# Kernel tuning notes

Hardware: AMD Instinct MI355X
Metric: run time of the kernel (lower is better)

Reference implementation:

```python
import jax, jax.numpy as jnp
import numpy as np

B, S, D = 4, 2048, 1024
H = 16
HD = D // H  # 64

def setup_inputs() -> dict:
    key = jax.random.key(0)
    k1, k2, k3 = jax.random.split(key, 3)
    x = jax.random.normal(k1, (B, S, D), dtype=jnp.float32)
    w_qkv = jax.random.normal(k2, (D, 3 * D), dtype=jnp.float32) * 0.02
    w_proj = jax.random.normal(k3, (D, D), dtype=jnp.float32) * 0.02
    return {"x": x, "w_qkv": w_qkv, "w_proj": w_proj}

def reference(x, w_qkv, w_proj):
    b, s, d = x.shape
    qkv = x @ w_qkv                                  # [b,s,3d]
    q, k, v = jnp.split(qkv, 3, axis=2)
    # [b,s,d] -> [b,h,s,hd]
    q = q.reshape(b, s, H, HD).transpose(0, 2, 1, 3)
    k = k.reshape(b, s, H, HD).transpose(0, 2, 1, 3)
    v = v.reshape(b, s, H, HD).transpose(0, 2, 1, 3)
    att = jnp.einsum('bhqd,bhkd->bhqk', q, k) / jnp.sqrt(jnp.float32(HD))
    causal = jnp.tril(jnp.ones((s, s), dtype=bool))
    att = jnp.where(causal[None, None], att, jnp.float32(-jnp.inf))
    att = jax.nn.softmax(att, axis=-1)
    y = jnp.einsum('bhqk,bhkd->bhqd', att, v)        # [b,h,s,hd]
    y = y.transpose(0, 2, 1, 3).reshape(b, s, d)
    return y @ w_proj
```

## Files before the change

kernel.cpp:

```cpp
#include <hip/hip_runtime.h>
#include <stdint.h>

typedef unsigned short u16;
typedef __attribute__((ext_vector_type(8))) short bf16x8;
typedef __attribute__((ext_vector_type(4))) float f32x4;

__device__ __forceinline__ u16 f2bf(float f) {
  union { float f; unsigned u; } v; v.f = f;
  unsigned r = v.u + 0x7fffu + ((v.u >> 16) & 1u);
  return (u16)(r >> 16);
}

__device__ __forceinline__ void async_copy16(u16* lds_dst, const u16* g_src) {
  __builtin_amdgcn_global_load_lds(
      (const __attribute__((address_space(1))) unsigned*)(g_src),
      (__attribute__((address_space(3))) unsigned*)(lds_dst),
      16, 0, 0);
}

__global__ void cvt_bf16_kernel(const float* __restrict__ in, u16* __restrict__ out, int n4) {
  int i = blockIdx.x * blockDim.x + threadIdx.x;
  int stride = gridDim.x * blockDim.x;
  for (; i < n4; i += stride) {
    float4 v = ((const float4*)in)[i];
    ushort4 o;
    o.x = f2bf(v.x); o.y = f2bf(v.y); o.z = f2bf(v.z); o.w = f2bf(v.w);
    ((ushort4*)out)[i] = o;
  }
}

__global__ void transpose_cvt_kernel(const float* __restrict__ in, u16* __restrict__ out,
                                     int R, int C) {
  __shared__ float tile[32][33];
  int bx = blockIdx.x * 32;
  int by = blockIdx.y * 32;
  int tx = threadIdx.x & 31, ty = threadIdx.x >> 5;
#pragma unroll
  for (int j = 0; j < 32; j += 8)
    tile[ty + j][tx] = in[(size_t)(by + ty + j) * C + bx + tx];
  __syncthreads();
#pragma unroll
  for (int j = 0; j < 32; j += 8)
    out[(size_t)(bx + ty + j) * R + by + tx] = f2bf(tile[tx][ty + j]);
}

template<int MODE>
__global__ __launch_bounds__(256, 2)
void gemm_bt(const u16* __restrict__ A, const u16* __restrict__ BT,
             int K, int N,
             u16* __restrict__ q_o, u16* __restrict__ k_o, u16* __restrict__ vt_o,
             float* __restrict__ f_o) {
  __shared__ u16 As[128 * 32];
  __shared__ u16 Bs[128 * 32];
  const int t = threadIdx.x;
  const int w = t >> 6, l = t & 63;
  const int lr = l & 15, lk = (l >> 4) * 8;
  const int m0 = blockIdx.x * 128, n0 = blockIdx.y * 128;
  const int wr = (w >> 1) * 64, wc = (w & 1) * 64;
  f32x4 acc[4][4] = {};
  const int row_s = t >> 2, seg_s = (t & 3) * 8;

  for (int kk = 0; kk < K; kk += 32) {
    async_copy16(&As[t * 8],         &A[(size_t)(m0 + row_s) * K + kk + seg_s]);
    async_copy16(&As[(t + 256) * 8], &A[(size_t)(m0 + row_s + 64) * K + kk + seg_s]);
    async_copy16(&Bs[t * 8],         &BT[(size_t)(n0 + row_s) * K + kk + seg_s]);
    async_copy16(&Bs[(t + 256) * 8], &BT[(size_t)(n0 + row_s + 64) * K + kk + seg_s]);
    __syncthreads();
    bf16x8 af[4], bfr[4];
#pragma unroll
    for (int mf = 0; mf < 4; ++mf)
      af[mf] = *(const bf16x8*)&As[(wr + mf * 16 + lr) * 32 + lk];
#pragma unroll
    for (int nf = 0; nf < 4; ++nf)
      bfr[nf] = *(const bf16x8*)&Bs[(wc + nf * 16 + lr) * 32 + lk];
#pragma unroll
    for (int mf = 0; mf < 4; ++mf)
#pragma unroll
      for (int nf = 0; nf < 4; ++nf)
        acc[mf][nf] = __builtin_amdgcn_mfma_f32_16x16x32_bf16(af[mf], bfr[nf], acc[mf][nf], 0, 0, 0);
    __syncthreads();
  }

#pragma unroll
  for (int mf = 0; mf < 4; ++mf) {
#pragma unroll
    for (int nf = 0; nf < 4; ++nf) {
      const int col = n0 + wc + nf * 16 + lr;
#pragma unroll
      for (int j = 0; j < 4; ++j) {
        const int row = m0 + wr + mf * 16 + ((l >> 4) << 2) + j;
        const float v = acc[mf][nf][j];
        if (MODE == 0) {
          const int which = col >> 10, r = col & 1023;
          const int h = r >> 6, hd = r & 63;
          const int b = row >> 11, s = row & 2047;
          const size_t bh = (size_t)b * 16 + h;
          if (which == 0)      q_o[(bh * 2048 + s) * 64 + hd] = f2bf(v * 0.125f);
          else if (which == 1) k_o[(bh * 2048 + s) * 64 + hd] = f2bf(v);
          else                 vt_o[(bh * 64 + hd) * 2048 + s] = f2bf(v);
        } else {
          f_o[(size_t)row * N + col] = v;
        }
      }
    }
  }
}

__global__ __launch_bounds__(256, 2)
void attn_kernel(const u16* __restrict__ qws, const u16* __restrict__ kws,
                 const u16* __restrict__ vtws, u16* __restrict__ ybf) {
  __shared__ u16 Ksh[2][64 * 64];
  __shared__ u16 VTsh[2][64 * 64];
  __shared__ u16 Psh[4][32 * 64];

  const int bh = blockIdx.x & 63;
  const int qtile = 15 - (blockIdx.x >> 6);
  const int t = threadIdx.x;
  const int w = t >> 6, l = t & 63;
  const int lr = l & 15, g = l >> 4;
  const int q0 = qtile * 128 + w * 32;

  bf16x8 qf[2][2];
#pragma unroll
  for (int mf = 0; mf < 2; ++mf) {
    const u16* qb = qws + ((size_t)bh * 2048 + q0 + mf * 16 + lr) * 64 + g * 8;
#pragma unroll
    for (int ks = 0; ks < 2; ++ks) qf[mf][ks] = *(const bf16x8*)(qb + ks * 32);
  }

  f32x4 oacc[2][4] = {};
  float lrun[2][4] = {};

  const int srow = t >> 3;
  const int ssw = ((t & 7) * 16) ^ ((srow & 7) << 4);
  const u16* kb0 = kws + ((size_t)bh * 2048 + srow) * 64 + (ssw >> 1);
  const u16* vb0 = vtws + ((size_t)bh * 64 + srow) * 2048 + (ssw >> 1);

#define STAGE(kv0, buf)                                                \
  do {                                                                 \
    async_copy16(&Ksh[buf][t * 8],          kb0 + (size_t)(kv0)*64);   \
    async_copy16(&Ksh[buf][(t + 256) * 8],  kb0 + (size_t)((kv0)+32)*64); \
    async_copy16(&VTsh[buf][t * 8],         vb0 + (kv0));              \
    async_copy16(&VTsh[buf][(t + 256) * 8], vb0 + (size_t)32*2048 + (kv0)); \
  } while (0)

  const int nt = (qtile + 1) * 2;
  STAGE(0, 0);
  __syncthreads();

  for (int ti = 0; ti < nt; ++ti) {
    const int kv0 = ti * 64;
    const int cur = ti & 1;
    if (ti + 1 < nt) STAGE((ti + 1) * 64, cur ^ 1);

    if (kv0 <= q0 + 31) {
      const u16* Kc = Ksh[cur];
      const u16* Vc = VTsh[cur];

      f32x4 s[2][4] = {};
      __builtin_amdgcn_s_setprio(1);
#pragma unroll
      for (int f = 0; f < 4; ++f) {
        const int krow = f * 16 + lr;
        const int kswz = (krow & 7) << 4;
#pragma unroll
        for (int ks = 0; ks < 2; ++ks) {
          bf16x8 kb = *(const bf16x8*)&Kc[krow * 64 + (((ks * 64 + g * 16) ^ kswz) >> 1)];
          s[0][f] = __builtin_amdgcn_mfma_f32_16x16x32_bf16(qf[0][ks], kb, s[0][f], 0, 0, 0);
          s[1][f] = __builtin_amdgcn_mfma_f32_16x16x32_bf16(qf[1][ks], kb, s[1][f], 0, 0, 0);
        }
      }
      __builtin_amdgcn_s_setprio(0);

      const bool diag = (kv0 + 63 > q0);
#pragma unroll
      for (int mf = 0; mf < 2; ++mf)
#pragma unroll
        for (int f = 0; f < 4; ++f)
#pragma unroll
          for (int j = 0; j < 4; ++j) {
            float p = __expf(s[mf][f][j]);
            if (diag) {
              const int key = kv0 + f * 16 + lr;
              const int qrow = q0 + mf * 16 + g * 4 + j;
              p = (key <= qrow) ? p : 0.f;
            }
            s[mf][f][j] = p;
            lrun[mf][j] += p;
          }

#pragma unroll
      for (int mf = 0; mf < 2; ++mf)
#pragma unroll
        for (int f = 0; f < 4; ++f)
#pragma unroll
          for (int j = 0; j < 4; ++j) {
            const int prow = mf * 16 + g * 4 + j;
            Psh[w][prow * 64 + (((f * 32 + lr * 2) ^ ((prow & 7) << 4)) >> 1)] =
                f2bf(s[mf][f][j]);
          }

#pragma unroll
      for (int ks = 0; ks < 2; ++ks) {
        bf16x8 pa[2];
#pragma unroll
        for (int mf = 0; mf < 2; ++mf) {
          const int prow = mf * 16 + lr;
          pa[mf] = *(const bf16x8*)&Psh[w][prow * 64 + (((ks * 64 + g * 16) ^ ((prow & 7) << 4)) >> 1)];
        }
        __builtin_amdgcn_s_setprio(1);
#pragma unroll
        for (int nf = 0; nf < 4; ++nf) {
          const int vrow = nf * 16 + lr;
          bf16x8 vb = *(const bf16x8*)&Vc[vrow * 64 + (((ks * 64 + g * 16) ^ ((vrow & 7) << 4)) >> 1)];
          oacc[0][nf] = __builtin_amdgcn_mfma_f32_16x16x32_bf16(pa[0], vb, oacc[0][nf], 0, 0, 0);
          oacc[1][nf] = __builtin_amdgcn_mfma_f32_16x16x32_bf16(pa[1], vb, oacc[1][nf], 0, 0, 0);
        }
        __builtin_amdgcn_s_setprio(0);
      }
    }
    __syncthreads();
  }
#undef STAGE

  float linv[2][4];
#pragma unroll
  for (int mf = 0; mf < 2; ++mf)
#pragma unroll
    for (int j = 0; j < 4; ++j) {
      float s = lrun[mf][j];
#pragma unroll
      for (int d = 1; d < 16; d <<= 1) s += __shfl_xor(s, d, 64);
      linv[mf][j] = 1.f / s;
    }

  const int b = bh >> 4, h = bh & 15;
#pragma unroll
  for (int mf = 0; mf < 2; ++mf)
#pragma unroll
    for (int nf = 0; nf < 4; ++nf) {
      const int col = nf * 16 + lr;
#pragma unroll
      for (int j = 0; j < 4; ++j) {
        const int row = q0 + mf * 16 + g * 4 + j;
        const float o = oacc[mf][nf][j] * linv[mf][j];
        ybf[((size_t)b * 2048 + row) * 1024 + h * 64 + col] = f2bf(o);
      }
    }
}

extern "C" void kernel_launch(void* const* d_in, const int* in_sizes, int n_in,
                              void* d_out, int out_size, void* d_ws, size_t ws_size,
                              hipStream_t stream) {
  const float* x     = (const float*)d_in[0];
  const float* wqkv  = (const float*)d_in[1];
  const float* wproj = (const float*)d_in[2];
  float* out = (float*)d_out;

  char* ws = (char*)d_ws;
  u16* xbf    = (u16*)ws;
  u16* ybf    = xbf;
  u16* wqkvT  = (u16*)(ws + 16777216);
  u16* wprojT = (u16*)(ws + 16777216 + 6291456);
  u16* qws    = (u16*)(ws + 25165824);
  u16* kws    = (u16*)(ws + 41943040);
  u16* vtws   = (u16*)(ws + 58720256);

  cvt_bf16_kernel<<<2048, 256, 0, stream>>>(x, xbf, (8192 * 1024) / 4);
  transpose_cvt_kernel<<<dim3(3072 / 32, 1024 / 32), 256, 0, stream>>>(wqkv, wqkvT, 1024, 3072);
  transpose_cvt_kernel<<<dim3(1024 / 32, 1024 / 32), 256, 0, stream>>>(wproj, wprojT, 1024, 1024);
  gemm_bt<0><<<dim3(64, 24), 256, 0, stream>>>(xbf, wqkvT, 1024, 3072, qws, kws, vtws, nullptr);
  attn_kernel<<<16 * 64, 256, 0, stream>>>(qws, kws, vtws, ybf);
  gemm_bt<1><<<dim3(64, 8), 256, 0, stream>>>(ybf, wprojT, 1024, 1024, nullptr, nullptr, nullptr, out);
}
```

Measured before the change: 188.5 us.

## Add 256x256-tile 8-wave pipelined GEMM for the QKV projection

Replaces the 128x128 single-stage QKV GEMM with a 512-thread kernel that computes 256x256 tiles. It uses a 64-wide K step, double-buffered swizzled LDS, and async global-to-LDS prefetch interleaved with MFMA phases under explicit barriers and waitcnts. The aim is higher data reuse per LDS load and overlap of memory traffic with matrix math. In exchange it needs 128KB of LDS per block, so occupancy drops to one block per CU. The 384-block grid also leaves a partial second wave. The output projection keeps the old kernel, which is simplified to its float-output path.

```diff
diff --git a/kernel.cpp b/kernel.cpp
--- a/kernel.cpp
+++ b/kernel.cpp
@@ -17,6 +17,8 @@
       (__attribute__((address_space(3))) unsigned*)(lds_dst),
       16, 0, 0);
 }
+
+#define MFMA16(a, b, c) __builtin_amdgcn_mfma_f32_16x16x32_bf16((a), (b), (c), 0, 0, 0)
 
 __global__ void cvt_bf16_kernel(const float* __restrict__ in, u16* __restrict__ out, int n4) {
   int i = blockIdx.x * blockDim.x + threadIdx.x;
@@ -45,11 +47,168 @@
 }
 
 template<int MODE>
+__global__ __launch_bounds__(512, 2)
+void gemm256(const u16* __restrict__ A, const u16* __restrict__ BT,
+             int N,
+             u16* __restrict__ q_o, u16* __restrict__ k_o, u16* __restrict__ vt_o,
+             float* __restrict__ f_o) {
+  constexpr int K = 1024;
+  constexpr int NT = K / 64;
+  __shared__ u16 AsF[2 * 2 * 8192];
+  __shared__ u16 BsF[2 * 2 * 8192];
+
+  const int t = threadIdx.x;
+  const int w = t >> 6, l = t & 63;
+  const int lr = l & 15, g = l >> 4;
+  const int wm = w >> 2, wn = w & 3;
+  const int m0 = blockIdx.x * 256, n0 = blockIdx.y * 256;
+
+  const int r = t >> 3;
+  const int sw = ((t & 7) * 16) ^ ((r & 7) << 4);
+  const u16* pA0 = A + (size_t)(m0 + r) * K + (sw >> 1);
+  const u16* pA1 = pA0 + (size_t)128 * K;
+  const u16* pB0 = BT + (size_t)(n0 + r) * K + (sw >> 1);
+  const u16* pB1 = pB0 + (size_t)128 * K;
+
+#define STG(ptr, dstbase)                                            \
+  do {                                                               \
+    async_copy16((dstbase) + t * 8, (ptr));                          \
+    async_copy16((dstbase) + 4096 + t * 8, (ptr) + (size_t)64 * K);  \
+  } while (0)
+
+  f32x4 acc[8][4] = {};
+
+  STG(pA0, AsF);
+  STG(pA1, AsF + 8192);
+  STG(pB0, BsF);
+  STG(pB1, BsF + 8192);
+  STG(pA0 + 64, AsF + 2 * 8192);
+  STG(pA1 + 64, AsF + 3 * 8192);
+  asm volatile("s_waitcnt vmcnt(4)" ::: "memory");
+  asm volatile("s_barrier" ::: "memory");
+
+  const int brow0 = (wn & 1) * 64;
+  for (int T = 0; T < NT; ++T) {
+    const int b = T & 1;
+    const u16* Ab = AsF + (b * 2 + wm) * 8192;
+    const u16* Bb = BsF + (b * 2 + (wn >> 1)) * 8192;
+    bf16x8 a03[4][2], a47[4][2], bb[4][2];
+
+#pragma unroll
+    for (int mf = 0; mf < 4; ++mf)
+#pragma unroll
+      for (int ks = 0; ks < 2; ++ks) {
+        const int row = mf * 16 + lr;
+        a03[mf][ks] = *(const bf16x8*)&Ab[row * 64 + (((ks * 64 + g * 16) ^ ((row & 7) << 4)) >> 1)];
+      }
+#pragma unroll
+    for (int nf = 0; nf < 2; ++nf)
+#pragma unroll
+      for (int ks = 0; ks < 2; ++ks) {
+        const int row = brow0 + nf * 16 + lr;
+        bb[nf][ks] = *(const bf16x8*)&Bb[row * 64 + (((ks * 64 + g * 16) ^ ((row & 7) << 4)) >> 1)];
+      }
+    if (T < NT - 1) STG(pB0 + (T + 1) * 64, BsF + ((T + 1) & 1) * 2 * 8192);
+    asm volatile("s_barrier" ::: "memory");
+    __builtin_amdgcn_s_setprio(1);
+#pragma unroll
+    for (int mf = 0; mf < 4; ++mf)
+#pragma unroll
+      for (int nf = 0; nf < 2; ++nf) {
+        acc[mf][nf] = MFMA16(a03[mf][0], bb[nf][0], acc[mf][nf]);
+        acc[mf][nf] = MFMA16(a03[mf][1], bb[nf][1], acc[mf][nf]);
+      }
+    __builtin_amdgcn_s_setprio(0);
+    asm volatile("s_barrier" ::: "memory");
+
+#pragma unroll
+    for (int mf = 0; mf < 4; ++mf)
+#pragma unroll
+      for (int ks = 0; ks < 2; ++ks) {
+        const int row = 64 + mf * 16 + lr;
+        a47[mf][ks] = *(const bf16x8*)&Ab[row * 64 + (((ks * 64 + g * 16) ^ ((row & 7) << 4)) >> 1)];
+      }
+#pragma unroll
+    for (int nf = 2; nf < 4; ++nf)
+#pragma unroll
+      for (int ks = 0; ks < 2; ++ks) {
+        const int row = brow0 + nf * 16 + lr;
+        bb[nf][ks] = *(const bf16x8*)&Bb[row * 64 + (((ks * 64 + g * 16) ^ ((row & 7) << 4)) >> 1)];
+      }
+    if (T < NT - 1) STG(pB1 + (T + 1) * 64, BsF + (((T + 1) & 1) * 2 + 1) * 8192);
+    asm volatile("s_barrier" ::: "memory");
+    __builtin_amdgcn_s_setprio(1);
+#pragma unroll
+    for (int mf = 0; mf < 4; ++mf)
+#pragma unroll
+      for (int nf = 2; nf < 4; ++nf) {
+        acc[mf][nf] = MFMA16(a03[mf][0], bb[nf][0], acc[mf][nf]);
+        acc[mf][nf] = MFMA16(a03[mf][1], bb[nf][1], acc[mf][nf]);
+      }
+    __builtin_amdgcn_s_setprio(0);
+    asm volatile("s_waitcnt lgkmcnt(0)" ::: "memory");
+    asm volatile("s_barrier" ::: "memory");
+
+    if (T < NT - 2) STG(pA0 + (T + 2) * 64, AsF + b * 2 * 8192);
+    asm volatile("s_barrier" ::: "memory");
+    __builtin_amdgcn_s_setprio(1);
+#pragma unroll
+    for (int mf = 0; mf < 4; ++mf)
+#pragma unroll
+      for (int nf = 0; nf < 2; ++nf) {
+        acc[4 + mf][nf] = MFMA16(a47[mf][0], bb[nf][0], acc[4 + mf][nf]);
+        acc[4 + mf][nf] = MFMA16(a47[mf][1], bb[nf][1], acc[4 + mf][nf]);
+      }
+    __builtin_amdgcn_s_setprio(0);
+    asm volatile("s_barrier" ::: "memory");
+
+    if (T < NT - 2) STG(pA1 + (T + 2) * 64, AsF + (b * 2 + 1) * 8192);
+    asm volatile("s_barrier" ::: "memory");
+    __builtin_amdgcn_s_setprio(1);
+#pragma unroll
+    for (int mf = 0; mf < 4; ++mf)
+#pragma unroll
+      for (int nf = 2; nf < 4; ++nf) {
+        acc[4 + mf][nf] = MFMA16(a47[mf][0], bb[nf][0], acc[4 + mf][nf]);
+        acc[4 + mf][nf] = MFMA16(a47[mf][1], bb[nf][1], acc[4 + mf][nf]);
+      }
+    __builtin_amdgcn_s_setprio(0);
+    if (T < NT - 2)
+      asm volatile("s_waitcnt vmcnt(4)" ::: "memory");
+    else if (T == NT - 2)
+      asm volatile("s_waitcnt vmcnt(0)" ::: "memory");
+    asm volatile("s_barrier" ::: "memory");
+  }
+#undef STG
+
+#pragma unroll
+  for (int mf = 0; mf < 8; ++mf) {
+#pragma unroll
+    for (int nf = 0; nf < 4; ++nf) {
+      const int col = n0 + wn * 64 + nf * 16 + lr;
+#pragma unroll
+      for (int j = 0; j < 4; ++j) {
+        const int row = m0 + wm * 128 + mf * 16 + g * 4 + j;
+        const float v = acc[mf][nf][j];
+        if (MODE == 0) {
+          const int which = col >> 10, rr = col & 1023;
+          const int h = rr >> 6, hd = rr & 63;
+          const int bb_ = row >> 11, s = row & 2047;
+          const size_t bh = (size_t)bb_ * 16 + h;
+          if (which == 0)      q_o[(bh * 2048 + s) * 64 + hd] = f2bf(v * 0.125f);
+          else if (which == 1) k_o[(bh * 2048 + s) * 64 + hd] = f2bf(v);
+          else                 vt_o[(bh * 64 + hd) * 2048 + s] = f2bf(v);
+        } else {
+          f_o[(size_t)row * N + col] = v;
+        }
+      }
+    }
+  }
+}
+
 __global__ __launch_bounds__(256, 2)
 void gemm_bt(const u16* __restrict__ A, const u16* __restrict__ BT,
-             int K, int N,
-             u16* __restrict__ q_o, u16* __restrict__ k_o, u16* __restrict__ vt_o,
-             float* __restrict__ f_o) {
+             int K, int N, float* __restrict__ f_o) {
   __shared__ u16 As[128 * 32];
   __shared__ u16 Bs[128 * 32];
   const int t = threadIdx.x;
@@ -77,33 +236,21 @@
     for (int mf = 0; mf < 4; ++mf)
 #pragma unroll
       for (int nf = 0; nf < 4; ++nf)
-        acc[mf][nf] = __builtin_amdgcn_mfma_f32_16x16x32_bf16(af[mf], bfr[nf], acc[mf][nf], 0, 0, 0);
+        acc[mf][nf] = MFMA16(af[mf], bfr[nf], acc[mf][nf]);
     __syncthreads();
   }
 
 #pragma unroll
-  for (int mf = 0; mf < 4; ++mf) {
+  for (int mf = 0; mf < 4; ++mf)
 #pragma unroll
     for (int nf = 0; nf < 4; ++nf) {
       const int col = n0 + wc + nf * 16 + lr;
 #pragma unroll
       for (int j = 0; j < 4; ++j) {
         const int row = m0 + wr + mf * 16 + ((l >> 4) << 2) + j;
-        const float v = acc[mf][nf][j];
-        if (MODE == 0) {
-          const int which = col >> 10, r = col & 1023;
-          const int h = r >> 6, hd = r & 63;
-          const int b = row >> 11, s = row & 2047;
-          const size_t bh = (size_t)b * 16 + h;
-          if (which == 0)      q_o[(bh * 2048 + s) * 64 + hd] = f2bf(v * 0.125f);
-          else if (which == 1) k_o[(bh * 2048 + s) * 64 + hd] = f2bf(v);
-          else                 vt_o[(bh * 64 + hd) * 2048 + s] = f2bf(v);
-        } else {
-          f_o[(size_t)row * N + col] = v;
-        }
+        f_o[(size_t)row * N + col] = acc[mf][nf][j];
       }
     }
-  }
 }
 
 __global__ __launch_bounds__(256, 2)
@@ -166,8 +313,8 @@
 #pragma unroll
         for (int ks = 0; ks < 2; ++ks) {
           bf16x8 kb = *(const bf16x8*)&Kc[krow * 64 + (((ks * 64 + g * 16) ^ kswz) >> 1)];
-          s[0][f] = __builtin_amdgcn_mfma_f32_16x16x32_bf16(qf[0][ks], kb, s[0][f], 0, 0, 0);
-          s[1][f] = __builtin_amdgcn_mfma_f32_16x16x32_bf16(qf[1][ks], kb, s[1][f], 0, 0, 0);
+          s[0][f] = MFMA16(qf[0][ks], kb, s[0][f]);
+          s[1][f] = MFMA16(qf[1][ks], kb, s[1][f]);
         }
       }
       __builtin_amdgcn_s_setprio(0);
@@ -213,8 +360,8 @@
         for (int nf = 0; nf < 4; ++nf) {
           const int vrow = nf * 16 + lr;
           bf16x8 vb = *(const bf16x8*)&Vc[vrow * 64 + (((ks * 64 + g * 16) ^ ((vrow & 7) << 4)) >> 1)];
-          oacc[0][nf] = __builtin_amdgcn_mfma_f32_16x16x32_bf16(pa[0], vb, oacc[0][nf], 0, 0, 0);
-          oacc[1][nf] = __builtin_amdgcn_mfma_f32_16x16x32_bf16(pa[1], vb, oacc[1][nf], 0, 0, 0);
+          oacc[0][nf] = MFMA16(pa[0], vb, oacc[0][nf]);
+          oacc[1][nf] = MFMA16(pa[1], vb, oacc[1][nf]);
         }
         __builtin_amdgcn_s_setprio(0);
       }
@@ -269,7 +416,7 @@
   cvt_bf16_kernel<<<2048, 256, 0, stream>>>(x, xbf, (8192 * 1024) / 4);
   transpose_cvt_kernel<<<dim3(3072 / 32, 1024 / 32), 256, 0, stream>>>(wqkv, wqkvT, 1024, 3072);
   transpose_cvt_kernel<<<dim3(1024 / 32, 1024 / 32), 256, 0, stream>>>(wproj, wprojT, 1024, 1024);
-  gemm_bt<0><<<dim3(64, 24), 256, 0, stream>>>(xbf, wqkvT, 1024, 3072, qws, kws, vtws, nullptr);
+  gemm256<0><<<dim3(32, 12), 512, 0, stream>>>(xbf, wqkvT, 3072, qws, kws, vtws, nullptr);
   attn_kernel<<<16 * 64, 256, 0, stream>>>(qws, kws, vtws, ybf);
-  gemm_bt<1><<<dim3(64, 8), 256, 0, stream>>>(ybf, wprojT, 1024, 1024, nullptr, nullptr, nullptr, out);
-}
+  gemm_bt<<<dim3(64, 8), 256, 0, stream>>>(ybf, wprojT, 1024, 1024, out);
+}
```

New measurement: 196.9 us. 4.5% more time.

## Double-buffer GEMM LDS tiles with K=64 stages and XOR-swizzled layout

Applied to the files above, without the earlier changes.

Rewrites the projection GEMM main loop to use two LDS buffers holding 64-wide K tiles, issuing the async global-to-LDS copy for the next tile while MFMAs run on the current one. This cuts the loop to one barrier per iteration instead of two and halves the iteration count. The shared tile is XOR-swizzled per row to avoid LDS bank conflicts on fragment reads. LDS use grows to 64KB per block, which may limit occupancy to the two blocks requested by the launch bounds.

```diff
diff --git a/kernel.cpp b/kernel.cpp
--- a/kernel.cpp
+++ b/kernel.cpp
@@ -17,6 +17,8 @@
       (__attribute__((address_space(3))) unsigned*)(lds_dst),
       16, 0, 0);
 }
+
+#define MFMA16(a, b, c) __builtin_amdgcn_mfma_f32_16x16x32_bf16((a), (b), (c), 0, 0, 0)
 
 __global__ void cvt_bf16_kernel(const float* __restrict__ in, u16* __restrict__ out, int n4) {
   int i = blockIdx.x * blockDim.x + threadIdx.x;
@@ -46,53 +48,84 @@
 
 template<int MODE>
 __global__ __launch_bounds__(256, 2)
-void gemm_bt(const u16* __restrict__ A, const u16* __restrict__ BT,
+void gemm2ph(const u16* __restrict__ A, const u16* __restrict__ BT,
              int K, int N,
              u16* __restrict__ q_o, u16* __restrict__ k_o, u16* __restrict__ vt_o,
              float* __restrict__ f_o) {
-  __shared__ u16 As[128 * 32];
-  __shared__ u16 Bs[128 * 32];
+  __shared__ u16 As[2][128 * 64];
+  __shared__ u16 Bs[2][128 * 64];
+
   const int t = threadIdx.x;
   const int w = t >> 6, l = t & 63;
-  const int lr = l & 15, lk = (l >> 4) * 8;
+  const int lr = l & 15, g = l >> 4;
+  const int wm = (w >> 1) * 64, wn = (w & 1) * 64;
   const int m0 = blockIdx.x * 128, n0 = blockIdx.y * 128;
-  const int wr = (w >> 1) * 64, wc = (w & 1) * 64;
+
+  const int r = t >> 3;
+  const int sw = ((t & 7) * 16) ^ ((r & 7) << 4);
+  const u16* pA = A + (size_t)(m0 + r) * K + (sw >> 1);
+  const u16* pB = BT + (size_t)(n0 + r) * K + (sw >> 1);
+
+#define STG(buf, kk)                                                    \
+  do {                                                                  \
+    async_copy16(&As[buf][t * 8],        pA + (kk));                    \
+    async_copy16(&As[buf][2048 + t * 8], pA + (size_t)32 * K + (kk));   \
+    async_copy16(&As[buf][4096 + t * 8], pA + (size_t)64 * K + (kk));   \
+    async_copy16(&As[buf][6144 + t * 8], pA + (size_t)96 * K + (kk));   \
+    async_copy16(&Bs[buf][t * 8],        pB + (kk));                    \
+    async_copy16(&Bs[buf][2048 + t * 8], pB + (size_t)32 * K + (kk));   \
+    async_copy16(&Bs[buf][4096 + t * 8], pB + (size_t)64 * K + (kk));   \
+    async_copy16(&Bs[buf][6144 + t * 8], pB + (size_t)96 * K + (kk));   \
+  } while (0)
+
   f32x4 acc[4][4] = {};
-  const int row_s = t >> 2, seg_s = (t & 3) * 8;
-
-  for (int kk = 0; kk < K; kk += 32) {
-    async_copy16(&As[t * 8],         &A[(size_t)(m0 + row_s) * K + kk + seg_s]);
-    async_copy16(&As[(t + 256) * 8], &A[(size_t)(m0 + row_s + 64) * K + kk + seg_s]);
-    async_copy16(&Bs[t * 8],         &BT[(size_t)(n0 + row_s) * K + kk + seg_s]);
-    async_copy16(&Bs[(t + 256) * 8], &BT[(size_t)(n0 + row_s + 64) * K + kk + seg_s]);
+
+  STG(0, 0);
+  __syncthreads();
+
+  const int NTt = K / 64;
+  for (int T = 0; T < NTt; ++T) {
+    const int cur = T & 1;
+    if (T + 1 < NTt) STG(cur ^ 1, (T + 1) * 64);
+
+    bf16x8 af[4][2], bfr[4][2];
+#pragma unroll
+    for (int mf = 0; mf < 4; ++mf)
+#pragma unroll
+      for (int ks = 0; ks < 2; ++ks) {
+        const int row = wm + mf * 16 + lr;
+        af[mf][ks] = *(const bf16x8*)&As[cur][row * 64 + (((ks * 64 + g * 16) ^ ((row & 7) << 4)) >> 1)];
+      }
+#pragma unroll
+    for (int nf = 0; nf < 4; ++nf)
+#pragma unroll
+      for (int ks = 0; ks < 2; ++ks) {
+        const int row = wn + nf * 16 + lr;
+        bfr[nf][ks] = *(const bf16x8*)&Bs[cur][row * 64 + (((ks * 64 + g * 16) ^ ((row & 7) << 4)) >> 1)];
+      }
+#pragma unroll
+    for (int mf = 0; mf < 4; ++mf)
+#pragma unroll
+      for (int nf = 0; nf < 4; ++nf) {
+        acc[mf][nf] = MFMA16(af[mf][0], bfr[nf][0], acc[mf][nf]);
+        acc[mf][nf] = MFMA16(af[mf][1], bfr[nf][1], acc[mf][nf]);
+      }
     __syncthreads();
-    bf16x8 af[4], bfr[4];
-#pragma unroll
-    for (int mf = 0; mf < 4; ++mf)
-      af[mf] = *(const bf16x8*)&As[(wr + mf * 16 + lr) * 32 + lk];
-#pragma unroll
-    for (int nf = 0; nf < 4; ++nf)
-      bfr[nf] = *(const bf16x8*)&Bs[(wc + nf * 16 + lr) * 32 + lk];
-#pragma unroll
-    for (int mf = 0; mf < 4; ++mf)
-#pragma unroll
-      for (int nf = 0; nf < 4; ++nf)
-        acc[mf][nf] = __builtin_amdgcn_mfma_f32_16x16x32_bf16(af[mf], bfr[nf], acc[mf][nf], 0, 0, 0);
-    __syncthreads();
-  }
+  }
+#undef STG
 
 #pragma unroll
   for (int mf = 0; mf < 4; ++mf) {
 #pragma unroll
     for (int nf = 0; nf < 4; ++nf) {
-      const int col = n0 + wc + nf * 16 + lr;
+      const int col = n0 + wn + nf * 16 + lr;
 #pragma unroll
       for (int j = 0; j < 4; ++j) {
-        const int row = m0 + wr + mf * 16 + ((l >> 4) << 2) + j;
+        const int row = m0 + wm + mf * 16 + g * 4 + j;
         const float v = acc[mf][nf][j];
         if (MODE == 0) {
-          const int which = col >> 10, r = col & 1023;
-          const int h = r >> 6, hd = r & 63;
+          const int which = col >> 10, rr = col & 1023;
+          const int h = rr >> 6, hd = rr & 63;
           const int b = row >> 11, s = row & 2047;
           const size_t bh = (size_t)b * 16 + h;
           if (which == 0)      q_o[(bh * 2048 + s) * 64 + hd] = f2bf(v * 0.125f);
@@ -166,8 +199,8 @@
 #pragma unroll
         for (int ks = 0; ks < 2; ++ks) {
           bf16x8 kb = *(const bf16x8*)&Kc[krow * 64 + (((ks * 64 + g * 16) ^ kswz) >> 1)];
-          s[0][f] = __builtin_amdgcn_mfma_f32_16x16x32_bf16(qf[0][ks], kb, s[0][f], 0, 0, 0);
-          s[1][f] = __builtin_amdgcn_mfma_f32_16x16x32_bf16(qf[1][ks], kb, s[1][f], 0, 0, 0);
+          s[0][f] = MFMA16(qf[0][ks], kb, s[0][f]);
+          s[1][f] = MFMA16(qf[1][ks], kb, s[1][f]);
         }
       }
       __builtin_amdgcn_s_setprio(0);
@@ -213,8 +246,8 @@
         for (int nf = 0; nf < 4; ++nf) {
           const int vrow = nf * 16 + lr;
           bf16x8 vb = *(const bf16x8*)&Vc[vrow * 64 + (((ks * 64 + g * 16) ^ ((vrow & 7) << 4)) >> 1)];
-          oacc[0][nf] = __builtin_amdgcn_mfma_f32_16x16x32_bf16(pa[0], vb, oacc[0][nf], 0, 0, 0);
-          oacc[1][nf] = __builtin_amdgcn_mfma_f32_16x16x32_bf16(pa[1], vb, oacc[1][nf], 0, 0, 0);
+          oacc[0][nf] = MFMA16(pa[0], vb, oacc[0][nf]);
+          oacc[1][nf] = MFMA16(pa[1], vb, oacc[1][nf]);
         }
         __builtin_amdgcn_s_setprio(0);
       }
@@ -269,7 +302,7 @@
   cvt_bf16_kernel<<<2048, 256, 0, stream>>>(x, xbf, (8192 * 1024) / 4);
   transpose_cvt_kernel<<<dim3(3072 / 32, 1024 / 32), 256, 0, stream>>>(wqkv, wqkvT, 1024, 3072);
   transpose_cvt_kernel<<<dim3(1024 / 32, 1024 / 32), 256, 0, stream>>>(wproj, wprojT, 1024, 1024);
-  gemm_bt<0><<<dim3(64, 24), 256, 0, stream>>>(xbf, wqkvT, 1024, 3072, qws, kws, vtws, nullptr);
+  gemm2ph<0><<<dim3(64, 24), 256, 0, stream>>>(xbf, wqkvT, 1024, 3072, qws, kws, vtws, nullptr);
   attn_kernel<<<16 * 64, 256, 0, stream>>>(qws, kws, vtws, ybf);
-  gemm_bt<1><<<dim3(64, 8), 256, 0, stream>>>(ybf, wprojT, 1024, 1024, nullptr, nullptr, nullptr, out);
-}
+  gemm2ph<1><<<dim3(64, 8), 256, 0, stream>>>(ybf, wprojT, 1024, 1024, nullptr, nullptr, nullptr, out);
+}
```

Result: faster. 183.1 us (-2.9%).
